# Performance work log

Measured on AMD Instinct MI355X. Metric: run time of the kernel, lower is better.

Reference implementation:

```python
import jax, jax.numpy as jnp
import numpy as np

B, H, S, DK = 4, 16, 2048, 128
NEG = -1e9  # large-negative stand-in for -inf additive mask
CAUSAL = True  # module constructed with mask=True (decoder self-attention)


def setup_inputs() -> dict:
    key = jax.random.key(0)
    kq, kk, kv, kl = jax.random.split(key, 4)
    q = jax.random.normal(kq, (B, H, S, DK), dtype=jnp.float32)
    k = jax.random.normal(kk, (B, H, S, DK), dtype=jnp.float32)
    v = jax.random.normal(kv, (B, H, S, DK), dtype=jnp.float32)
    sen_len = jax.random.randint(kl, (B,), 1, S + 1, dtype=jnp.int32)
    return {"q": q, "k": k, "v": v, "sen_len": sen_len}


def reference(q, k, v, sen_len):
    # att = q @ k^T / sqrt(d)   -> (B, H, S, S)
    scale = 1.0 / jnp.sqrt(jnp.asarray(DK, dtype=q.dtype))
    att = jnp.einsum('bhqd,bhkd->bhqk', q, k) * scale

    # Fused padding (+ optional causal) mask, multiplicative zero-mask and
    # additive -inf mask, exactly as att*zero_mask + inf_mask in the original.
    pos = jnp.arange(S)
    valid = pos[None, :] < sen_len[:, None]                 # (B, S) token validity
    zmask = (valid[:, :, None] & valid[:, None, :])         # (B, S, S) pad mask
    if CAUSAL:
        zmask = zmask & (pos[None, :, None] >= pos[None, None, :])
    zmask = zmask[:, None, :, :].astype(att.dtype)          # (B, 1, S, S)
    att = att * zmask + NEG * (1.0 - zmask)

    att = jax.nn.softmax(att, axis=-1)
    return jnp.einsum('bhqk,bhkd->bhqd', att, v)
```

## Files before the change

### kernel.cpp

```cpp
#include <hip/hip_runtime.h>
#include <hip/hip_bf16.h>

#define Bb   4
#define Hh   16
#define Ss   2048
#define Dd   128
#define QBLK 128
#define KVB  64
#define NW   4

typedef __attribute__((ext_vector_type(8))) short bf16x8;
typedef __attribute__((ext_vector_type(4))) float f32x4;
typedef __attribute__((ext_vector_type(4))) float fvec4;
typedef __attribute__((ext_vector_type(2))) unsigned u32x2;
typedef __attribute__((ext_vector_type(4))) unsigned u32x4;

__device__ __forceinline__ unsigned pk2(float a, float b) {
    __hip_bfloat162 h = __float22bfloat162_rn(make_float2(a, b));
    unsigned u; __builtin_memcpy(&u, &h, 4); return u;
}

typedef const __attribute__((address_space(1))) char* gas_t;
typedef __attribute__((address_space(3))) char* las_t;
__device__ __forceinline__ void gld16(const void* g, void* l) {
    __builtin_amdgcn_global_load_lds((gas_t)g, (las_t)l, 16, 0, 0);
}

__global__ __launch_bounds__(256) void cvtk_kernel(const float* __restrict__ K,
                                                   short* __restrict__ Kb) {
    size_t i = ((size_t)blockIdx.x * 256 + threadIdx.x) * 8;
    fvec4 a = ((const fvec4*)(K + i))[0];
    fvec4 b = ((const fvec4*)(K + i))[1];
    u32x4 u;
    u[0] = pk2(a[0], a[1]); u[1] = pk2(a[2], a[3]);
    u[2] = pk2(b[0], b[1]); u[3] = pk2(b[2], b[3]);
    *(u32x4*)(Kb + i) = u;
}

__global__ __launch_bounds__(256) void cvtv_kernel(const float* __restrict__ V,
                                                   short* __restrict__ Vt,
                                                   float* __restrict__ part) {
    __shared__ short Lt[128 * 136];
    __shared__ fvec4 red[256];
    const int bh = blockIdx.x >> 4, ch = blockIdx.x & 15;
    const int tid = threadIdx.x;
    const float* src = V + ((size_t)bh * Ss + ch * 128) * Dd;
    const int c4 = tid & 31, s0 = tid >> 5;
    fvec4 acc = {0.f, 0.f, 0.f, 0.f};
    #pragma unroll
    for (int i = 0; i < 16; ++i) {
        int s = s0 + 8 * i;
        fvec4 v = ((const fvec4*)(src + (size_t)s * Dd))[c4];
        acc += v;
        u32x2 p; p[0] = pk2(v[0], v[1]); p[1] = pk2(v[2], v[3]);
        *(u32x2*)&Lt[s * 136 + c4 * 4] = p;
    }
    red[tid] = acc;
    __syncthreads();
    for (int off = 128; off >= 32; off >>= 1) {
        if (tid < off) red[tid] += red[tid + off];
        __syncthreads();
    }
    if (tid < 32) ((fvec4*)(part + (size_t)blockIdx.x * Dd))[tid] = red[tid];
    #pragma unroll
    for (int i = 0; i < 8; ++i) {
        int g2 = tid + 256 * i;
        int d = g2 >> 4, sg = g2 & 15;
        short tmp[8];
        #pragma unroll
        for (int j = 0; j < 8; ++j) tmp[j] = Lt[(sg * 8 + j) * 136 + d];
        u32x4 u; __builtin_memcpy(&u, tmp, 16);
        *(u32x4*)(Vt + ((size_t)(bh * Dd + d)) * Ss + ch * 128 + sg * 8) = u;
    }
}

__global__ __launch_bounds__(256) void vpart_kernel(const float* __restrict__ V,
                                                    float* __restrict__ part) {
    int blk = blockIdx.x, bh = blk >> 3, ch = blk & 7;
    int tid = threadIdx.x, d4 = tid & 31, rg = tid >> 5;
    const fvec4* p = (const fvec4*)(V + ((size_t)bh * Ss + ch * 256) * Dd) + d4;
    fvec4 s = {0.f, 0.f, 0.f, 0.f};
    for (int rr = 0; rr < 32; ++rr) s += p[(size_t)(rg * 32 + rr) * 32];
    __shared__ fvec4 red[256];
    red[tid] = s;
    __syncthreads();
    for (int off = 128; off >= 32; off >>= 1) {
        if (tid < off) red[tid] += red[tid + off];
        __syncthreads();
    }
    if (tid < 32) ((fvec4*)(part + (size_t)blk * Dd))[tid] = red[tid];
}

__global__ __launch_bounds__(128) void vcomb_kernel(const float* __restrict__ part,
                                                    float* __restrict__ vm, int nch) {
    int bh = blockIdx.x, d = threadIdx.x;
    float s = 0.f;
    for (int c = 0; c < nch; ++c) s += part[(size_t)(bh * nch + c) * Dd + d];
    vm[bh * Dd + d] = s * (1.0f / 2048.0f);
}

template<int MODE>
__global__ __launch_bounds__(256, 2) void attn_kernel(
    const float* __restrict__ Qg, const float* __restrict__ Kg,
    const float* __restrict__ Vg, const short* __restrict__ Kbf,
    const short* __restrict__ Vtb, const int* __restrict__ slen,
    const float* __restrict__ vmean, float* __restrict__ Og)
{
    __shared__ __align__(16) short Ks[2][KVB * Dd];
    __shared__ __align__(16) short Vt[2][Dd * KVB];
    __shared__ __align__(16) short Ps[NW * 32 * KVB];

    const int bid = blockIdx.x;
    const int qslot = bid >> 6, r = bid & 63;
    const int qt = 15 - qslot;
    const int b  = (r >> 3) & 3;
    const int h  = (r & 7) | ((r >> 5) << 3);
    const int bh = b * 16 + h;
    const int len = slen[b];
    const int q0 = qt * QBLK;
    const int tid = threadIdx.x;

    if (q0 >= len) {
        const fvec4* vm4 = (const fvec4*)(vmean + bh * Dd);
        fvec4 val = vm4[tid & 31];
        float* ob = Og + ((size_t)bh * Ss + q0) * Dd;
        int r0 = tid >> 5;
        #pragma unroll
        for (int i = 0; i < 16; ++i)
            ((fvec4*)(ob + (size_t)(r0 + 8 * i) * Dd))[tid & 31] = val;
        return;
    }

    const int w = tid >> 6, lane = tid & 63;
    const int g = lane >> 4, qc = lane & 15;
    const int qw0 = q0 + w * 32;
    const bool wave_active = (qw0 < len);

    const int kv_end   = min(q0 + QBLK, len);
    const int kv_end_w = min(qw0 + 32, kv_end);
    const int nt = (kv_end + KVB - 1) >> 6;

    int CK[4], CV[4];
    const char* KbhB = (const char*)Kbf + (size_t)bh * Ss * 256;
    const char* VbhB = (const char*)Vtb + (size_t)bh * Dd * (Ss * 2);
    if constexpr (MODE == 0) {
        #pragma unroll
        for (int i = 0; i < 4; ++i) {
            int krow = w * 16 + i * 4 + (lane >> 4);
            int jK = lane & 15;
            int jKs = (jK & 8) | ((jK & 7) ^ (krow & 7));
            CK[i] = krow * 256 + jKs * 16;
            int d = w * 32 + i * 8 + (lane >> 3);
            int jV = lane & 7;
            CV[i] = d * 4096 + (jV ^ (d & 7)) * 16;
        }
    }

    #define GISSUE(tile_, bf_) do {                                                    \
        size_t kb_ = (size_t)(tile_) * (KVB * 256);                                    \
        size_t vb_ = (size_t)(tile_) * (KVB * 2);                                      \
        _Pragma("unroll")                                                              \
        for (int i_ = 0; i_ < 4; ++i_)                                                 \
            gld16(KbhB + kb_ + CK[i_], (char*)Ks[bf_] + w * 4096 + i_ * 1024);         \
        _Pragma("unroll")                                                              \
        for (int i_ = 0; i_ < 4; ++i_)                                                 \
            gld16(VbhB + vb_ + CV[i_], (char*)Vt[bf_] + w * 4096 + i_ * 1024);         \
    } while (0)

    #define STAGE_CVT(kv0_) do {                                                       \
        const fvec4* sk_ = (const fvec4*)(Kg + ((size_t)bh * Ss + (kv0_)) * Dd);       \
        _Pragma("unroll")                                                              \
        for (int i_ = 0; i_ < 8; ++i_) {                                               \
            int f_ = tid + 256 * i_;                                                   \
            int kr_ = f_ >> 5, d4_ = f_ & 31;                                          \
            fvec4 v_ = sk_[(size_t)kr_ * 32 + d4_];                                    \
            u32x2 pr_; pr_[0] = pk2(v_[0], v_[1]); pr_[1] = pk2(v_[2], v_[3]);         \
            int j_ = d4_ >> 1;                                                         \
            int js_ = (j_ & 8) | ((j_ & 7) ^ (kr_ & 7));                               \
            *(u32x2*)((char*)Ks[0] + kr_ * 256 + js_ * 16 + (d4_ & 1) * 8) = pr_;      \
        }                                                                              \
        const float* sv_ = Vg + ((size_t)bh * Ss + (kv0_)) * Dd;                       \
        _Pragma("unroll")                                                              \
        for (int i_ = 0; i_ < 2; ++i_) {                                               \
            int idx_ = tid + 256 * i_;                                                 \
            int dt4_ = idx_ & 31, kt4_ = idx_ >> 5;                                    \
            fvec4 vv_[4];                                                              \
            _Pragma("unroll")                                                          \
            for (int jj_ = 0; jj_ < 4; ++jj_)                                          \
                vv_[jj_] = ((const fvec4*)(sv_ + (size_t)(kt4_ * 4 + jj_) * Dd))[dt4_];\
            _Pragma("unroll")                                                          \
            for (int jj_ = 0; jj_ < 4; ++jj_) {                                        \
                int d_ = dt4_ * 4 + jj_;                                               \
                u32x2 pr_;                                                             \
                pr_[0] = pk2(vv_[0][jj_], vv_[1][jj_]);                                \
                pr_[1] = pk2(vv_[2][jj_], vv_[3][jj_]);                                \
                int bo_ = d_ * 128 + ((kt4_ >> 1) ^ (d_ & 7)) * 16 + (kt4_ & 1) * 8;   \
                *(u32x2*)((char*)Vt[0] + bo_) = pr_;                                   \
            }                                                                          \
        }                                                                              \
    } while (0)

    if constexpr (MODE == 0) GISSUE(0, 0);

    const float SC = 0.12752870368768582f;
    bf16x8 qf[2][4];
    #pragma unroll
    for (int t2 = 0; t2 < 2; ++t2) {
        const float* qrow = Qg + ((size_t)bh * Ss + (qw0 + 16 * t2 + qc)) * Dd;
        #pragma unroll
        for (int kc = 0; kc < 4; ++kc) {
            const fvec4* p = (const fvec4*)(qrow + kc * 32 + g * 8);
            fvec4 a = p[0], bv = p[1];
            unsigned* fu = (unsigned*)&qf[t2][kc];
            fu[0] = pk2(a[0] * SC, a[1] * SC);
            fu[1] = pk2(a[2] * SC, a[3] * SC);
            fu[2] = pk2(bv[0] * SC, bv[1] * SC);
            fu[3] = pk2(bv[2] * SC, bv[3] * SC);
        }
    }

    if constexpr (MODE == 0) {
        asm volatile("s_waitcnt vmcnt(0)" ::: "memory");
        __syncthreads();
    }

    f32x4 o[2][8];
    #pragma unroll
    for (int t2 = 0; t2 < 2; ++t2)
        #pragma unroll
        for (int dt = 0; dt < 8; ++dt) o[t2][dt] = (f32x4){0.f, 0.f, 0.f, 0.f};
    float m_[2]   = {-3e38f, -3e38f};
    float lsum[2] = {0.f, 0.f};

    char* PsB = (char*)Ps + w * 4096;

    for (int t = 0; t < nt; ++t) {
        const int kv0 = t * KVB;
        const int cur = (MODE == 0) ? (t & 1) : 0;
        const bool pre = (t + 1 < nt);
        const bool active = wave_active && (kv0 < kv_end_w);

        if constexpr (MODE == 0) {
            if (pre) GISSUE(t + 1, (t & 1) ^ 1);
        } else {
            __syncthreads();
            STAGE_CVT(kv0);
            __syncthreads();
        }

        if (active) {
            const char* KsB = (const char*)Ks[cur];
            const char* VtB = (const char*)Vt[cur];
            f32x4 sa[2][4];
            #pragma unroll
            for (int t2 = 0; t2 < 2; ++t2)
                #pragma unroll
                for (int mt = 0; mt < 4; ++mt) sa[t2][mt] = (f32x4){0.f, 0.f, 0.f, 0.f};
            __builtin_amdgcn_s_setprio(1);
            #pragma unroll
            for (int mt = 0; mt < 4; ++mt) {
                int row = mt * 16 + qc;
                bf16x8 kf[4];
                #pragma unroll
                for (int kc = 0; kc < 4; ++kc) {
                    int jb = kc * 4 + g;
                    int js = (jb & 8) | ((jb & 7) ^ (row & 7));
                    kf[kc] = *(const bf16x8*)(KsB + row * 256 + js * 16);
                }
                #pragma unroll
                for (int t2 = 0; t2 < 2; ++t2)
                    #pragma unroll
                    for (int kc = 0; kc < 4; ++kc)
                        sa[t2][mt] = __builtin_amdgcn_mfma_f32_16x16x32_bf16(
                            kf[kc], qf[t2][kc], sa[t2][mt], 0, 0, 0);
            }
            __builtin_amdgcn_s_setprio(0);

            #pragma unroll
            for (int t2 = 0; t2 < 2; ++t2) {
                const int qrow = qw0 + 16 * t2 + qc;
                const bool full = (kv0 + KVB - 1) <= (qw0 + 16 * t2);
                if (!full) {
                    #pragma unroll
                    for (int mt = 0; mt < 4; ++mt)
                        #pragma unroll
                        for (int rr = 0; rr < 4; ++rr) {
                            int kk = kv0 + mt * 16 + g * 4 + rr;
                            if (kk > qrow) sa[t2][mt][rr] = -3e38f;
                        }
                }
                float tm = sa[t2][0][0];
                #pragma unroll
                for (int mt = 0; mt < 4; ++mt)
                    #pragma unroll
                    for (int rr = 0; rr < 4; ++rr) tm = fmaxf(tm, sa[t2][mt][rr]);
                tm = fmaxf(tm, __shfl_xor(tm, 16));
                tm = fmaxf(tm, __shfl_xor(tm, 32));
                if (__any(tm > m_[t2] + 8.0f)) {
                    float mnew = fmaxf(m_[t2], tm);
                    float al = exp2f(m_[t2] - mnew);
                    m_[t2] = mnew;
                    lsum[t2] *= al;
                    #pragma unroll
                    for (int rr = 0; rr < 4; ++rr) {
                        float alr = __shfl(al, g * 4 + rr);
                        #pragma unroll
                        for (int dt = 0; dt < 8; ++dt) o[t2][dt][rr] *= alr;
                    }
                }
                float mref = m_[t2];
                float ls = 0.f;
                int prow = t2 * 16 + qc;
                int pswz = (prow & 7) << 4;
                #pragma unroll
                for (int mt = 0; mt < 4; ++mt) {
                    f32x4 p;
                    #pragma unroll
                    for (int rr = 0; rr < 4; ++rr)
                        p[rr] = exp2f(sa[t2][mt][rr] - mref);
                    ls += (p[0] + p[1]) + (p[2] + p[3]);
                    u32x2 pw;
                    pw[0] = pk2(p[0], p[1]);
                    pw[1] = pk2(p[2], p[3]);
                    *(u32x2*)(PsB + ((prow * 128 + mt * 32 + g * 8) ^ pswz)) = pw;
                }
                lsum[t2] += ls;
            }

            bf16x8 ap[2][2];
            #pragma unroll
            for (int t2 = 0; t2 < 2; ++t2) {
                int prow = t2 * 16 + qc;
                int pswz = (prow & 7) << 4;
                #pragma unroll
                for (int c = 0; c < 2; ++c)
                    ap[t2][c] = *(const bf16x8*)(PsB + ((prow * 128 + c * 64 + g * 16) ^ pswz));
            }
            __builtin_amdgcn_s_setprio(1);
            #pragma unroll
            for (int dt = 0; dt < 8; ++dt) {
                int d = dt * 16 + qc;
                #pragma unroll
                for (int c = 0; c < 2; ++c) {
                    int js = (c * 4 + g) ^ (d & 7);
                    bf16x8 bfv = *(const bf16x8*)(VtB + d * 128 + js * 16);
                    #pragma unroll
                    for (int t2 = 0; t2 < 2; ++t2)
                        o[t2][dt] = __builtin_amdgcn_mfma_f32_16x16x32_bf16(
                            ap[t2][c], bfv, o[t2][dt], 0, 0, 0);
                }
            }
            __builtin_amdgcn_s_setprio(0);
        }

        if constexpr (MODE == 0) {
            if (pre) {
                asm volatile("s_waitcnt vmcnt(0)" ::: "memory");
                __syncthreads();
            }
        }
    }

    float inv_[2][4];
    #pragma unroll
    for (int t2 = 0; t2 < 2; ++t2) {
        float L = lsum[t2];
        L += __shfl_xor(L, 16);
        L += __shfl_xor(L, 32);
        #pragma unroll
        for (int rr = 0; rr < 4; ++rr) {
            float Lr = __shfl(L, g * 4 + rr);
            inv_[t2][rr] = 1.0f / Lr;
        }
    }
    bool needvm = (qw0 + 32 > len);
    float vmv[8];
    #pragma unroll
    for (int dt = 0; dt < 8; ++dt)
        vmv[dt] = needvm ? vmean[bh * Dd + dt * 16 + qc] : 0.f;
    #pragma unroll
    for (int t2 = 0; t2 < 2; ++t2)
        #pragma unroll
        for (int rr = 0; rr < 4; ++rr) {
            int rowg = qw0 + t2 * 16 + g * 4 + rr;
            float* orow = Og + ((size_t)bh * Ss + rowg) * Dd + qc;
            #pragma unroll
            for (int dt = 0; dt < 8; ++dt) {
                float val = o[t2][dt][rr] * inv_[t2][rr];
                if (rowg >= len) val = vmv[dt];
                orow[dt * 16] = val;
            }
        }
    #undef GISSUE
    #undef STAGE_CVT
}

extern "C" void kernel_launch(void* const* d_in, const int* in_sizes, int n_in,
                              void* d_out, int out_size, void* d_ws, size_t ws_size,
                              hipStream_t stream) {
    const float* q  = (const float*)d_in[0];
    const float* k  = (const float*)d_in[1];
    const float* v  = (const float*)d_in[2];
    const int*   sl = (const int*)d_in[3];
    float* out = (float*)d_out;

    const size_t nElem = (size_t)Bb * Hh * Ss * Dd;
    const size_t need0 = nElem * 2 * 2 + 1024 * Dd * 4 + 64 * Dd * 4;

    if (ws_size >= need0) {
        short* Kbf  = (short*)d_ws;
        short* Vtb  = Kbf + nElem;
        float* part = (float*)(Vtb + nElem);
        float* vm   = part + 1024 * Dd;
        cvtk_kernel<<<dim3(8192), dim3(256), 0, stream>>>(k, Kbf);
        cvtv_kernel<<<dim3(1024), dim3(256), 0, stream>>>(v, Vtb, part);
        vcomb_kernel<<<dim3(Bb * Hh), dim3(128), 0, stream>>>(part, vm, 16);
        attn_kernel<0><<<dim3(1024), dim3(256), 0, stream>>>(q, k, v, Kbf, Vtb, sl, vm, out);
    } else {
        float* part = (float*)d_ws;
        float* vm   = part + 512 * Dd;
        vpart_kernel<<<dim3(512), dim3(256), 0, stream>>>(v, part);
        vcomb_kernel<<<dim3(Bb * Hh), dim3(128), 0, stream>>>(part, vm, 8);
        attn_kernel<1><<<dim3(1024), dim3(256), 0, stream>>>(q, k, v, (const short*)nullptr,
                                                             (const short*)nullptr, sl, vm, out);
    }
}
```

Baseline: 136.7 us.

## Split KV tiles across two wave groups per block and merge softmax partials

The attention kernel now runs 8 waves per block in two groups of four. The groups take alternating KV tiles, each with its own double-buffered LDS region. At the end, group 1 writes its partial O, max and sum to LDS, and group 0 merges them with rescaled online-softmax math before writing the output. This is meant to shorten the serial KV loop per query tile, so the long causal rows finish sooner and the tail is better balanced. In exchange the block uses 160KB of LDS, which limits occupancy to one block per CU, and adds a merge step with extra syncs. The fallback path is split into its own non-templated kernel.

```diff
diff --git a/kernel.cpp b/kernel.cpp
--- a/kernel.cpp
+++ b/kernel.cpp
@@ -7,7 +7,6 @@
 #define Dd   128
 #define QBLK 128
 #define KVB  64
-#define NW   4
 
 typedef __attribute__((ext_vector_type(8))) short bf16x8;
 typedef __attribute__((ext_vector_type(4))) float f32x4;
@@ -99,16 +98,12 @@
     vm[bh * Dd + d] = s * (1.0f / 2048.0f);
 }
 
-template<int MODE>
-__global__ __launch_bounds__(256, 2) void attn_kernel(
-    const float* __restrict__ Qg, const float* __restrict__ Kg,
-    const float* __restrict__ Vg, const short* __restrict__ Kbf,
+__global__ __launch_bounds__(512, 2) void attn8_kernel(
+    const float* __restrict__ Qg, const short* __restrict__ Kbf,
     const short* __restrict__ Vtb, const int* __restrict__ slen,
     const float* __restrict__ vmean, float* __restrict__ Og)
 {
-    __shared__ __align__(16) short Ks[2][KVB * Dd];
-    __shared__ __align__(16) short Vt[2][Dd * KVB];
-    __shared__ __align__(16) short Ps[NW * 32 * KVB];
+    __shared__ __align__(16) char smem[163840];
 
     const int bid = blockIdx.x;
     const int qslot = bid >> 6, r = bid & 63;
@@ -126,81 +121,52 @@
         float* ob = Og + ((size_t)bh * Ss + q0) * Dd;
         int r0 = tid >> 5;
         #pragma unroll
-        for (int i = 0; i < 16; ++i)
-            ((fvec4*)(ob + (size_t)(r0 + 8 * i) * Dd))[tid & 31] = val;
+        for (int i = 0; i < 8; ++i)
+            ((fvec4*)(ob + (size_t)(r0 + 16 * i) * Dd))[tid & 31] = val;
         return;
     }
 
     const int w = tid >> 6, lane = tid & 63;
+    const int grp = w >> 2, wg = w & 3;
     const int g = lane >> 4, qc = lane & 15;
-    const int qw0 = q0 + w * 32;
+    const int qw0 = q0 + wg * 32;
     const bool wave_active = (qw0 < len);
 
     const int kv_end   = min(q0 + QBLK, len);
     const int kv_end_w = min(qw0 + 32, kv_end);
-    const int nt = (kv_end + KVB - 1) >> 6;
+    const int nt  = (kv_end + KVB - 1) >> 6;
+    const int itn = (nt + 1) >> 1;
+
+    char* const KgB = smem + grp * 32768;
+    char* const VgB = smem + 65536 + grp * 32768;
+    char* const PsB = smem + 131072 + w * 4096;
 
     int CK[4], CV[4];
     const char* KbhB = (const char*)Kbf + (size_t)bh * Ss * 256;
     const char* VbhB = (const char*)Vtb + (size_t)bh * Dd * (Ss * 2);
-    if constexpr (MODE == 0) {
-        #pragma unroll
-        for (int i = 0; i < 4; ++i) {
-            int krow = w * 16 + i * 4 + (lane >> 4);
-            int jK = lane & 15;
-            int jKs = (jK & 8) | ((jK & 7) ^ (krow & 7));
-            CK[i] = krow * 256 + jKs * 16;
-            int d = w * 32 + i * 8 + (lane >> 3);
-            int jV = lane & 7;
-            CV[i] = d * 4096 + (jV ^ (d & 7)) * 16;
-        }
-    }
-
-    #define GISSUE(tile_, bf_) do {                                                    \
+    #pragma unroll
+    for (int i = 0; i < 4; ++i) {
+        int krow = wg * 16 + i * 4 + (lane >> 4);
+        int jK = lane & 15;
+        int jKs = (jK & 8) | ((jK & 7) ^ (krow & 7));
+        CK[i] = krow * 256 + jKs * 16;
+        int d = wg * 32 + i * 8 + (lane >> 3);
+        int jV = lane & 7;
+        CV[i] = d * 4096 + (jV ^ (d & 7)) * 16;
+    }
+
+    #define GISSUE8(tile_, buf_) do {                                                  \
         size_t kb_ = (size_t)(tile_) * (KVB * 256);                                    \
         size_t vb_ = (size_t)(tile_) * (KVB * 2);                                      \
         _Pragma("unroll")                                                              \
         for (int i_ = 0; i_ < 4; ++i_)                                                 \
-            gld16(KbhB + kb_ + CK[i_], (char*)Ks[bf_] + w * 4096 + i_ * 1024);         \
+            gld16(KbhB + kb_ + CK[i_], KgB + (buf_) * 16384 + wg * 4096 + i_ * 1024);  \
         _Pragma("unroll")                                                              \
         for (int i_ = 0; i_ < 4; ++i_)                                                 \
-            gld16(VbhB + vb_ + CV[i_], (char*)Vt[bf_] + w * 4096 + i_ * 1024);         \
+            gld16(VbhB + vb_ + CV[i_], VgB + (buf_) * 16384 + wg * 4096 + i_ * 1024);  \
     } while (0)
 
-    #define STAGE_CVT(kv0_) do {                                                       \
-        const fvec4* sk_ = (const fvec4*)(Kg + ((size_t)bh * Ss + (kv0_)) * Dd);       \
-        _Pragma("unroll")                                                              \
-        for (int i_ = 0; i_ < 8; ++i_) {                                               \
-            int f_ = tid + 256 * i_;                                                   \
-            int kr_ = f_ >> 5, d4_ = f_ & 31;                                          \
-            fvec4 v_ = sk_[(size_t)kr_ * 32 + d4_];                                    \
-            u32x2 pr_; pr_[0] = pk2(v_[0], v_[1]); pr_[1] = pk2(v_[2], v_[3]);         \
-            int j_ = d4_ >> 1;                                                         \
-            int js_ = (j_ & 8) | ((j_ & 7) ^ (kr_ & 7));                               \
-            *(u32x2*)((char*)Ks[0] + kr_ * 256 + js_ * 16 + (d4_ & 1) * 8) = pr_;      \
-        }                                                                              \
-        const float* sv_ = Vg + ((size_t)bh * Ss + (kv0_)) * Dd;                       \
-        _Pragma("unroll")                                                              \
-        for (int i_ = 0; i_ < 2; ++i_) {                                               \
-            int idx_ = tid + 256 * i_;                                                 \
-            int dt4_ = idx_ & 31, kt4_ = idx_ >> 5;                                    \
-            fvec4 vv_[4];                                                              \
-            _Pragma("unroll")                                                          \
-            for (int jj_ = 0; jj_ < 4; ++jj_)                                          \
-                vv_[jj_] = ((const fvec4*)(sv_ + (size_t)(kt4_ * 4 + jj_) * Dd))[dt4_];\
-            _Pragma("unroll")                                                          \
-            for (int jj_ = 0; jj_ < 4; ++jj_) {                                        \
-                int d_ = dt4_ * 4 + jj_;                                               \
-                u32x2 pr_;                                                             \
-                pr_[0] = pk2(vv_[0][jj_], vv_[1][jj_]);                                \
-                pr_[1] = pk2(vv_[2][jj_], vv_[3][jj_]);                                \
-                int bo_ = d_ * 128 + ((kt4_ >> 1) ^ (d_ & 7)) * 16 + (kt4_ & 1) * 8;   \
-                *(u32x2*)((char*)Vt[0] + bo_) = pr_;                                   \
-            }                                                                          \
-        }                                                                              \
-    } while (0)
-
-    if constexpr (MODE == 0) GISSUE(0, 0);
+    if (grp < nt) GISSUE8(grp, 0);
 
     const float SC = 0.12752870368768582f;
     bf16x8 qf[2][4];
@@ -219,10 +185,8 @@
         }
     }
 
-    if constexpr (MODE == 0) {
-        asm volatile("s_waitcnt vmcnt(0)" ::: "memory");
-        __syncthreads();
-    }
+    asm volatile("s_waitcnt vmcnt(0)" ::: "memory");
+    __syncthreads();
 
     f32x4 o[2][8];
     #pragma unroll
@@ -232,25 +196,17 @@
     float m_[2]   = {-3e38f, -3e38f};
     float lsum[2] = {0.f, 0.f};
 
-    char* PsB = (char*)Ps + w * 4096;
-
-    for (int t = 0; t < nt; ++t) {
+    for (int i = 0; i < itn; ++i) {
+        const int t = 2 * i + grp;
         const int kv0 = t * KVB;
-        const int cur = (MODE == 0) ? (t & 1) : 0;
-        const bool pre = (t + 1 < nt);
-        const bool active = wave_active && (kv0 < kv_end_w);
-
-        if constexpr (MODE == 0) {
-            if (pre) GISSUE(t + 1, (t & 1) ^ 1);
-        } else {
-            __syncthreads();
-            STAGE_CVT(kv0);
-            __syncthreads();
-        }
+        const int tn = t + 2;
+        const bool active = wave_active && (t < nt) && (kv0 < kv_end_w);
+
+        if (tn < nt) GISSUE8(tn, (i + 1) & 1);
 
         if (active) {
-            const char* KsB = (const char*)Ks[cur];
-            const char* VtB = (const char*)Vt[cur];
+            const char* KsB = KgB + (i & 1) * 16384;
+            const char* VtB = VgB + (i & 1) * 16384;
             f32x4 sa[2][4];
             #pragma unroll
             for (int t2 = 0; t2 < 2; ++t2)
@@ -353,10 +309,267 @@
             __builtin_amdgcn_s_setprio(0);
         }
 
-        if constexpr (MODE == 0) {
-            if (pre) {
-                asm volatile("s_waitcnt vmcnt(0)" ::: "memory");
-                __syncthreads();
+        asm volatile("s_waitcnt vmcnt(0)" ::: "memory");
+        __syncthreads();
+    }
+    #undef GISSUE8
+
+    __syncthreads();
+    float* dumpO  = (float*)smem;
+    float* dumpML = (float*)(smem + 65536);
+    if (grp == 1) {
+        #pragma unroll
+        for (int t2 = 0; t2 < 2; ++t2) {
+            float L = lsum[t2];
+            L += __shfl_xor(L, 16);
+            L += __shfl_xor(L, 32);
+            if (lane < 16) {
+                dumpML[wg * 64 + t2 * 32 + qc * 2 + 0] = m_[t2];
+                dumpML[wg * 64 + t2 * 32 + qc * 2 + 1] = L;
+            }
+            #pragma unroll
+            for (int dt = 0; dt < 8; ++dt)
+                *(f32x4*)(dumpO + wg * 4096 + (t2 * 8 + dt) * 256 + lane * 4) = o[t2][dt];
+        }
+    }
+    __syncthreads();
+    if (grp == 1) return;
+
+    bool needvm = (qw0 + 32 > len);
+    float vmv[8];
+    #pragma unroll
+    for (int dt = 0; dt < 8; ++dt)
+        vmv[dt] = needvm ? vmean[bh * Dd + dt * 16 + qc] : 0.f;
+
+    #pragma unroll
+    for (int t2 = 0; t2 < 2; ++t2) {
+        float mB = dumpML[wg * 64 + t2 * 32 + qc * 2 + 0];
+        float lB = dumpML[wg * 64 + t2 * 32 + qc * 2 + 1];
+        float LA = lsum[t2];
+        LA += __shfl_xor(LA, 16);
+        LA += __shfl_xor(LA, 32);
+        float mM = fmaxf(m_[t2], mB);
+        float aA = exp2f(m_[t2] - mM);
+        float aB = exp2f(mB - mM);
+        float invL = 1.0f / (LA * aA + lB * aB);
+        f32x4 obv[8];
+        #pragma unroll
+        for (int dt = 0; dt < 8; ++dt)
+            obv[dt] = *(const f32x4*)(dumpO + wg * 4096 + (t2 * 8 + dt) * 256 + lane * 4);
+        #pragma unroll
+        for (int rr = 0; rr < 4; ++rr) {
+            float aAr = __shfl(aA, g * 4 + rr);
+            float aBr = __shfl(aB, g * 4 + rr);
+            float ivr = __shfl(invL, g * 4 + rr);
+            int rowg = qw0 + t2 * 16 + g * 4 + rr;
+            float* orow = Og + ((size_t)bh * Ss + rowg) * Dd + qc;
+            #pragma unroll
+            for (int dt = 0; dt < 8; ++dt) {
+                float val = (o[t2][dt][rr] * aAr + obv[dt][rr] * aBr) * ivr;
+                if (rowg >= len) val = vmv[dt];
+                orow[dt * 16] = val;
+            }
+        }
+    }
+}
+
+__global__ __launch_bounds__(256, 2) void attn_fb_kernel(
+    const float* __restrict__ Qg, const float* __restrict__ Kg,
+    const float* __restrict__ Vg, const int* __restrict__ slen,
+    const float* __restrict__ vmean, float* __restrict__ Og)
+{
+    __shared__ __align__(16) short Ks[KVB * Dd];
+    __shared__ __align__(16) short Vt[Dd * KVB];
+    __shared__ __align__(16) short Ps[4 * 32 * KVB];
+
+    const int bid = blockIdx.x;
+    const int qslot = bid >> 6, r = bid & 63;
+    const int qt = 15 - qslot;
+    const int b  = (r >> 3) & 3;
+    const int h  = (r & 7) | ((r >> 5) << 3);
+    const int bh = b * 16 + h;
+    const int len = slen[b];
+    const int q0 = qt * QBLK;
+    const int tid = threadIdx.x;
+
+    if (q0 >= len) {
+        const fvec4* vm4 = (const fvec4*)(vmean + bh * Dd);
+        fvec4 val = vm4[tid & 31];
+        float* ob = Og + ((size_t)bh * Ss + q0) * Dd;
+        int r0 = tid >> 5;
+        #pragma unroll
+        for (int i = 0; i < 16; ++i)
+            ((fvec4*)(ob + (size_t)(r0 + 8 * i) * Dd))[tid & 31] = val;
+        return;
+    }
+
+    const int w = tid >> 6, lane = tid & 63;
+    const int g = lane >> 4, qc = lane & 15;
+    const int qw0 = q0 + w * 32;
+    const bool wave_active = (qw0 < len);
+
+    const int kv_end   = min(q0 + QBLK, len);
+    const int kv_end_w = min(qw0 + 32, kv_end);
+    const int nt = (kv_end + KVB - 1) >> 6;
+
+    const float SC = 0.12752870368768582f;
+    bf16x8 qf[2][4];
+    #pragma unroll
+    for (int t2 = 0; t2 < 2; ++t2) {
+        const float* qrow = Qg + ((size_t)bh * Ss + (qw0 + 16 * t2 + qc)) * Dd;
+        #pragma unroll
+        for (int kc = 0; kc < 4; ++kc) {
+            const fvec4* p = (const fvec4*)(qrow + kc * 32 + g * 8);
+            fvec4 a = p[0], bv = p[1];
+            unsigned* fu = (unsigned*)&qf[t2][kc];
+            fu[0] = pk2(a[0] * SC, a[1] * SC);
+            fu[1] = pk2(a[2] * SC, a[3] * SC);
+            fu[2] = pk2(bv[0] * SC, bv[1] * SC);
+            fu[3] = pk2(bv[2] * SC, bv[3] * SC);
+        }
+    }
+
+    f32x4 o[2][8];
+    #pragma unroll
+    for (int t2 = 0; t2 < 2; ++t2)
+        #pragma unroll
+        for (int dt = 0; dt < 8; ++dt) o[t2][dt] = (f32x4){0.f, 0.f, 0.f, 0.f};
+    float m_[2]   = {-3e38f, -3e38f};
+    float lsum[2] = {0.f, 0.f};
+    char* PsB = (char*)Ps + w * 4096;
+
+    for (int t = 0; t < nt; ++t) {
+        const int kv0 = t * KVB;
+        const bool active = wave_active && (kv0 < kv_end_w);
+        __syncthreads();
+        {
+            const fvec4* sk = (const fvec4*)(Kg + ((size_t)bh * Ss + kv0) * Dd);
+            #pragma unroll
+            for (int i = 0; i < 8; ++i) {
+                int f = tid + 256 * i;
+                int kr = f >> 5, d4 = f & 31;
+                fvec4 v = sk[(size_t)kr * 32 + d4];
+                u32x2 pr; pr[0] = pk2(v[0], v[1]); pr[1] = pk2(v[2], v[3]);
+                int j = d4 >> 1;
+                int js = (j & 8) | ((j & 7) ^ (kr & 7));
+                *(u32x2*)((char*)Ks + kr * 256 + js * 16 + (d4 & 1) * 8) = pr;
+            }
+            const float* sv = Vg + ((size_t)bh * Ss + kv0) * Dd;
+            #pragma unroll
+            for (int i = 0; i < 2; ++i) {
+                int idx = tid + 256 * i;
+                int dt4 = idx & 31, kt4 = idx >> 5;
+                fvec4 vv[4];
+                #pragma unroll
+                for (int jj = 0; jj < 4; ++jj)
+                    vv[jj] = ((const fvec4*)(sv + (size_t)(kt4 * 4 + jj) * Dd))[dt4];
+                #pragma unroll
+                for (int jj = 0; jj < 4; ++jj) {
+                    int d = dt4 * 4 + jj;
+                    u32x2 pr;
+                    pr[0] = pk2(vv[0][jj], vv[1][jj]);
+                    pr[1] = pk2(vv[2][jj], vv[3][jj]);
+                    int bo = d * 128 + ((kt4 >> 1) ^ (d & 7)) * 16 + (kt4 & 1) * 8;
+                    *(u32x2*)((char*)Vt + bo) = pr;
+                }
+            }
+        }
+        __syncthreads();
+
+        if (active) {
+            f32x4 sa[2][4];
+            #pragma unroll
+            for (int t2 = 0; t2 < 2; ++t2)
+                #pragma unroll
+                for (int mt = 0; mt < 4; ++mt) sa[t2][mt] = (f32x4){0.f, 0.f, 0.f, 0.f};
+            #pragma unroll
+            for (int mt = 0; mt < 4; ++mt) {
+                int row = mt * 16 + qc;
+                bf16x8 kf[4];
+                #pragma unroll
+                for (int kc = 0; kc < 4; ++kc) {
+                    int jb = kc * 4 + g;
+                    int js = (jb & 8) | ((jb & 7) ^ (row & 7));
+                    kf[kc] = *(const bf16x8*)((const char*)Ks + row * 256 + js * 16);
+                }
+                #pragma unroll
+                for (int t2 = 0; t2 < 2; ++t2)
+                    #pragma unroll
+                    for (int kc = 0; kc < 4; ++kc)
+                        sa[t2][mt] = __builtin_amdgcn_mfma_f32_16x16x32_bf16(
+                            kf[kc], qf[t2][kc], sa[t2][mt], 0, 0, 0);
+            }
+            #pragma unroll
+            for (int t2 = 0; t2 < 2; ++t2) {
+                const int qrow = qw0 + 16 * t2 + qc;
+                const bool full = (kv0 + KVB - 1) <= (qw0 + 16 * t2);
+                if (!full) {
+                    #pragma unroll
+                    for (int mt = 0; mt < 4; ++mt)
+                        #pragma unroll
+                        for (int rr = 0; rr < 4; ++rr) {
+                            int kk = kv0 + mt * 16 + g * 4 + rr;
+                            if (kk > qrow) sa[t2][mt][rr] = -3e38f;
+                        }
+                }
+                float tm = sa[t2][0][0];
+                #pragma unroll
+                for (int mt = 0; mt < 4; ++mt)
+                    #pragma unroll
+                    for (int rr = 0; rr < 4; ++rr) tm = fmaxf(tm, sa[t2][mt][rr]);
+                tm = fmaxf(tm, __shfl_xor(tm, 16));
+                tm = fmaxf(tm, __shfl_xor(tm, 32));
+                if (__any(tm > m_[t2] + 8.0f)) {
+                    float mnew = fmaxf(m_[t2], tm);
+                    float al = exp2f(m_[t2] - mnew);
+                    m_[t2] = mnew;
+                    lsum[t2] *= al;
+                    #pragma unroll
+                    for (int rr = 0; rr < 4; ++rr) {
+                        float alr = __shfl(al, g * 4 + rr);
+                        #pragma unroll
+                        for (int dt = 0; dt < 8; ++dt) o[t2][dt][rr] *= alr;
+                    }
+                }
+                float mref = m_[t2];
+                float ls = 0.f;
+                int prow = t2 * 16 + qc;
+                int pswz = (prow & 7) << 4;
+                #pragma unroll
+                for (int mt = 0; mt < 4; ++mt) {
+                    f32x4 p;
+                    #pragma unroll
+                    for (int rr = 0; rr < 4; ++rr)
+                        p[rr] = exp2f(sa[t2][mt][rr] - mref);
+                    ls += (p[0] + p[1]) + (p[2] + p[3]);
+                    u32x2 pw;
+                    pw[0] = pk2(p[0], p[1]);
+                    pw[1] = pk2(p[2], p[3]);
+                    *(u32x2*)(PsB + ((prow * 128 + mt * 32 + g * 8) ^ pswz)) = pw;
+                }
+                lsum[t2] += ls;
+            }
+            bf16x8 ap[2][2];
+            #pragma unroll
+            for (int t2 = 0; t2 < 2; ++t2) {
+                int prow = t2 * 16 + qc;
+                int pswz = (prow & 7) << 4;
+                #pragma unroll
+                for (int c = 0; c < 2; ++c)
+                    ap[t2][c] = *(const bf16x8*)(PsB + ((prow * 128 + c * 64 + g * 16) ^ pswz));
+            }
+            #pragma unroll
+            for (int dt = 0; dt < 8; ++dt) {
+                int d = dt * 16 + qc;
+                #pragma unroll
+                for (int c = 0; c < 2; ++c) {
+                    int js = (c * 4 + g) ^ (d & 7);
+                    bf16x8 bfv = *(const bf16x8*)((const char*)Vt + d * 128 + js * 16);
+                    #pragma unroll
+                    for (int t2 = 0; t2 < 2; ++t2)
+                        o[t2][dt] = __builtin_amdgcn_mfma_f32_16x16x32_bf16(
+                            ap[t2][c], bfv, o[t2][dt], 0, 0, 0);
+                }
             }
         }
     }
@@ -391,8 +604,6 @@
                 orow[dt * 16] = val;
             }
         }
-    #undef GISSUE
-    #undef STAGE_CVT
 }
 
 extern "C" void kernel_launch(void* const* d_in, const int* in_sizes, int n_in,
@@ -415,13 +626,12 @@
         cvtk_kernel<<<dim3(8192), dim3(256), 0, stream>>>(k, Kbf);
         cvtv_kernel<<<dim3(1024), dim3(256), 0, stream>>>(v, Vtb, part);
         vcomb_kernel<<<dim3(Bb * Hh), dim3(128), 0, stream>>>(part, vm, 16);
-        attn_kernel<0><<<dim3(1024), dim3(256), 0, stream>>>(q, k, v, Kbf, Vtb, sl, vm, out);
+        attn8_kernel<<<dim3(1024), dim3(512), 0, stream>>>(q, Kbf, Vtb, sl, vm, out);
     } else {
         float* part = (float*)d_ws;
         float* vm   = part + 512 * Dd;
         vpart_kernel<<<dim3(512), dim3(256), 0, stream>>>(v, part);
         vcomb_kernel<<<dim3(Bb * Hh), dim3(128), 0, stream>>>(part, vm, 8);
-        attn_kernel<1><<<dim3(1024), dim3(256), 0, stream>>>(q, k, v, (const short*)nullptr,
-                                                             (const short*)nullptr, sl, vm, out);
-    }
-}
+        attn_fb_kernel<<<dim3(1024), dim3(256), 0, stream>>>(q, k, v, sl, vm, out);
+    }
+}
```

Result: slower. 154.4 us (+12.9%).
